# Kernel optimization log

Hardware: AMD Instinct MI355X
Metric: run time of the kernel (lower is better)

## Reference

```python
import jax, jax.numpy as jnp
import numpy as np

GRID_SIZE = 5
NUM_BASES = 2 ** GRID_SIZE - 1  # 31: actual number of Haar bases produced by the loop

def _haar_edges():
    left, mid, right = [], [], []
    for level in range(GRID_SIZE):
        scale = 2 ** level
        for shift in range(scale):
            left.append(shift / scale)
            mid.append((shift + 0.5) / scale)
            right.append((shift + 1.0) / scale)
    return (np.asarray(left, np.float32), np.asarray(mid, np.float32), np.asarray(right, np.float32))

_LEFT, _MID, _RIGHT = _haar_edges()


def setup_inputs() -> dict:
    key = jax.random.key(0)
    k1, k2, k3 = jax.random.split(key, 3)
    B, IN, OUT = 16384, 256, 256
    x = jax.random.normal(k1, (B, IN), dtype=jnp.float32)
    base_weight = jax.random.normal(k2, (OUT, IN), dtype=jnp.float32) * 0.05
    spline_weight = jax.random.normal(k3, (OUT, IN, NUM_BASES), dtype=jnp.float32) * 0.05
    spline_scaler = jnp.ones((OUT, IN), dtype=jnp.float32)
    return {"x": x, "base_weight": base_weight, "spline_weight": spline_weight, "spline_scaler": spline_scaler}


def reference(x, base_weight, spline_weight, spline_scaler):
    # per-feature min/max normalization over the batch dim
    x_min = jnp.min(x, axis=0, keepdims=True)
    x_max = jnp.max(x, axis=0, keepdims=True)
    xn = (x - x_min) / (x_max - x_min + 1e-8)            # [B, IN]
    left = jnp.asarray(_LEFT, x.dtype)
    mid = jnp.asarray(_MID, x.dtype)
    right = jnp.asarray(_RIGHT, x.dtype)
    xe = xn[..., None]                                    # [B, IN, 1]
    mask1 = ((xe >= left) & (xe < mid)).astype(x.dtype)
    mask2 = ((xe >= mid) & (xe < right)).astype(x.dtype)
    bases = mask1 - mask2                                 # [B, IN, NB]
    base_out = jax.nn.relu(x) @ base_weight.T             # [B, OUT]
    sw = spline_weight * spline_scaler[..., None]         # [OUT, IN, NB]
    wavelet_out = jnp.einsum('bik,oik->bo', bases, sw)    # [B, OUT]
    return base_out + wavelet_out
```

## Files before the change

kernel.cpp:

```cpp
#include <hip/hip_runtime.h>
#include <stdint.h>

typedef short s16x8 __attribute__((ext_vector_type(8)));
typedef float f32x4 __attribute__((ext_vector_type(4)));

#define IN_F   256
#define OUT_F  256
#define BATCH  16384
#define NB     31
#define KONE   8192
#define KTOT   8448

typedef const __attribute__((address_space(1))) void* as1cvp;
typedef __attribute__((address_space(3))) void* as3vp;

__device__ __forceinline__ unsigned short f2bf(float f) {
    unsigned u = __float_as_uint(f);
    u += 0x7FFFu + ((u >> 16) & 1u);
    return (unsigned short)(u >> 16);
}
__device__ __forceinline__ unsigned fkey(float f) {
    unsigned b = __float_as_uint(f);
    return (b & 0x80000000u) ? ~b : (b | 0x80000000u);
}
__device__ __forceinline__ float funkey(unsigned k) {
    return __uint_as_float((k & 0x80000000u) ? (k & 0x7FFFFFFFu) : ~k);
}

__global__ void minmax_atomic(const float* __restrict__ x,
                              unsigned* __restrict__ pminP, unsigned* __restrict__ pmaxP) {
    const int t = threadIdx.x;
    const int b0 = blockIdx.x * 32;
    float mn = 3.4e38f, mx = -3.4e38f;
    for (int r = 0; r < 32; ++r) {
        float v = x[(size_t)(b0 + r) * IN_F + t];
        mn = fminf(mn, v);
        mx = fmaxf(mx, v);
    }
    atomicMin(&pminP[t], fkey(mn));
    atomicMax(&pmaxP[t], fkey(mx));
}

__global__ void build_wb(const float* __restrict__ bw, const float* __restrict__ sw,
                         const float* __restrict__ sc, unsigned short* __restrict__ Wb) {
    const int o = blockIdx.x;
    const int k0 = blockIdx.y * 2112;
    const int t = threadIdx.x;
    for (int k = k0 + t; k < k0 + 2112; k += 256) {
        float val;
        if (k < KONE) {
            int i = k >> 5, j = k & 31;
            float s = sc[o * IN_F + i];
            float acc = 0.f;
#pragma unroll
            for (int l = 0; l < 5; ++l) {
                int kk = (1 << l) - 1 + (j >> (5 - l));
                float w = sw[((size_t)(o * IN_F + i)) * NB + kk];
                acc += (((j >> (4 - l)) & 1) ? -w : w);
            }
            val = acc * s;
        } else {
            val = bw[o * IN_F + (k - KONE)];
        }
        Wb[(size_t)o * KTOT + k] = f2bf(val);
    }
}

__global__ __launch_bounds__(256) void leafk_t(
    const float* __restrict__ x, const unsigned* __restrict__ pminP,
    const unsigned* __restrict__ pmaxP, unsigned char* __restrict__ lt) {
    __shared__ unsigned char lsh[256 * 68];
    __shared__ float xminsh[IN_F], rdensh[IN_F];
    const int t = threadIdx.x;
    const int b0 = blockIdx.x * 64;
    {
        float mn = funkey(pminP[t]), mx = funkey(pmaxP[t]);
        xminsh[t] = mn;
        rdensh[t] = 1.0f / (mx - mn + 1e-8f);
    }
    __syncthreads();
    const float xmn = xminsh[t], rdn = rdensh[t];
    for (int r = 0; r < 64; ++r) {
        float v = x[(size_t)(b0 + r) * IN_F + t];
        float xn = (v - xmn) * rdn;
        int l = (int)(xn * 32.0f);
        lsh[t * 68 + r] = (l >= 0 && l < 32) ? (unsigned char)l : (unsigned char)255;
    }
    __syncthreads();
    const int lane = t & 63, w = t >> 6;
    const unsigned* lshU = (const unsigned*)lsh;
#pragma unroll
    for (int ib = 0; ib < 16; ++ib) {
        int i = ib * 16 + w * 4 + (lane >> 4);
        unsigned val = lshU[i * 17 + (lane & 15)];
        *(unsigned*)(lt + (size_t)i * BATCH + b0 + (lane & 15) * 4) = val;
    }
}

__global__ __launch_bounds__(128, 2) void gemm_kan(
    const float* __restrict__ x,
    const unsigned short* __restrict__ Wb,
    const unsigned char* __restrict__ lt,
    float* __restrict__ out)
{
    __shared__ unsigned short Ash[64 * 64];
    __shared__ unsigned short Bsh[2 * 64 * 64];

    const int t     = threadIdx.x;
    const int lane  = t & 63;
    const int wv    = t >> 6;
    const int mtile = blockIdx.x;
    const int ntile = blockIdx.y;

    {
        uint4 z; z.x = z.y = z.z = z.w = 0u;
        uint4* a4 = (uint4*)Ash;
#pragma unroll
        for (int r = 0; r < 4; ++r) a4[t + r * 128] = z;
    }

    const unsigned char* bbase = (const unsigned char*)(Wb
        + (size_t)(ntile * 64 + wv * 32 + (lane >> 3)) * KTOT
        + (((lane & 7) ^ (lane >> 3)) << 3));

    const int am = t >> 1;
    const int ag = t & 1;
    const size_t lrow0 = (size_t)mtile * 64;
    int ps = -1;

    unsigned char lf = lt[(size_t)ag * BATCH + lrow0 + am];

#pragma unroll
    for (int q = 0; q < 4; ++q)
        __builtin_amdgcn_global_load_lds(
            (as1cvp)(bbase + (size_t)q * 8 * KTOT * 2),
            (as3vp)(uint32_t)(uintptr_t)(Bsh + wv * 2048 + q * 512), 16, 0, 0);
    __syncthreads();

    f32x4 acc[2][4] = {};
    const int rr = lane & 15, kq = lane >> 4;

    for (int kb = 0; kb < 132; ++kb) {
        const int cur = kb & 1;
        if (kb < 128) {
            if (ps >= 0) Ash[ps] = 0;
            int l = lf;
            if (l < 32) {
                int c = (ag << 2) + (l >> 3);
                ps = (am << 6) + ((c ^ (am & 7)) << 3) + (l & 7);
                Ash[ps] = 0x3F80;
            } else ps = -1;
        } else {
            const float* xr = x + (size_t)(mtile * 64 + wv * 32) * IN_F + (kb - 128) * 64 + lane;
            const int cslot = (lane >> 3);
#pragma unroll
            for (int m0 = 0; m0 < 32; ++m0) {
                int m = wv * 32 + m0;
                float v = xr[(size_t)m0 * IN_F];
                Ash[(m << 6) + ((cslot ^ (m & 7)) << 3) + (lane & 7)] = f2bf(fmaxf(v, 0.0f));
            }
        }
        __syncthreads();

        if (kb + 1 < 132) {
            const unsigned char* src = bbase + (size_t)(kb + 1) * 128;
            unsigned short* dst = Bsh + (1 - cur) * 4096 + wv * 2048;
#pragma unroll
            for (int q = 0; q < 4; ++q)
                __builtin_amdgcn_global_load_lds(
                    (as1cvp)(src + (size_t)q * 8 * KTOT * 2),
                    (as3vp)(uint32_t)(uintptr_t)(dst + q * 512), 16, 0, 0);
        }
        if (kb + 1 < 128) {
            lf = lt[(size_t)((kb + 1) * 2 + ag) * BATCH + lrow0 + am];
        }

        const unsigned short* bb = Bsh + cur * 4096;
#pragma unroll
        for (int ks = 0; ks < 2; ++ks) {
            const int c = (ks << 2) + kq;
            s16x8 af[2], bfr[4];
#pragma unroll
            for (int mt = 0; mt < 2; ++mt) {
                int m = wv * 32 + mt * 16 + rr;
                af[mt] = *(const s16x8*)&Ash[(m << 6) + ((c ^ (m & 7)) << 3)];
            }
#pragma unroll
            for (int nt = 0; nt < 4; ++nt) {
                int n = nt * 16 + rr;
                bfr[nt] = *(const s16x8*)&bb[(n << 6) + ((c ^ (n & 7)) << 3)];
            }
#pragma unroll
            for (int mt = 0; mt < 2; ++mt)
#pragma unroll
                for (int nt = 0; nt < 4; ++nt)
                    acc[mt][nt] = __builtin_amdgcn_mfma_f32_16x16x32_bf16(
                        af[mt], bfr[nt], acc[mt][nt], 0, 0, 0);
        }
        __syncthreads();
    }

    const int rq = lane >> 4;
#pragma unroll
    for (int mt = 0; mt < 2; ++mt)
#pragma unroll
        for (int nt = 0; nt < 4; ++nt)
#pragma unroll
            for (int v = 0; v < 4; ++v) {
                int row = mtile * 64 + wv * 32 + mt * 16 + rq * 4 + v;
                int col = ntile * 64 + nt * 16 + rr;
                out[(size_t)row * OUT_F + col] = acc[mt][nt][v];
            }
}

extern "C" void kernel_launch(void* const* d_in, const int* in_sizes, int n_in,
                              void* d_out, int out_size, void* d_ws, size_t ws_size,
                              hipStream_t stream) {
    (void)in_sizes; (void)n_in; (void)out_size; (void)ws_size;
    const float* x  = (const float*)d_in[0];
    const float* bw = (const float*)d_in[1];
    const float* sw = (const float*)d_in[2];
    const float* sc = (const float*)d_in[3];
    float* out = (float*)d_out;

    char* ws = (char*)d_ws;
    unsigned short* Wb   = (unsigned short*)ws;
    unsigned char*  lt   = (unsigned char*)(ws + 4325376);
    unsigned*       pminP = (unsigned*)(ws + 8519680);
    unsigned*       pmaxP = (unsigned*)(ws + 8520704);

    hipMemsetAsync(pminP, 0xFF, 1024, stream);
    hipMemsetAsync(pmaxP, 0x00, 1024, stream);

    minmax_atomic<<<512, 256, 0, stream>>>(x, pminP, pmaxP);
    build_wb<<<dim3(256, 4), 256, 0, stream>>>(bw, sw, sc, Wb);
    leafk_t<<<256, 256, 0, stream>>>(x, pminP, pmaxP, lt);
    gemm_kan<<<dim3(256, 4), 128, 0, stream>>>(x, Wb, lt, out);
}
```

Before: 179.6 us.

## Build one-hot A fragments in registers, split K across blocks with atomics

The GEMM no longer stages the one-hot A matrix in shared memory. Each lane builds its bf16 one-hot fragment directly in registers from the leaf index, and the ReLU(x) part is loaded straight from global memory into registers. The K dimension is split over two blocks per output tile, with results accumulated into a zeroed output through float atomicAdd, and occupancy is raised to 4 blocks per SIMD. The atomic min/max over batch is replaced by a two-pass partial reduction that writes per-block partials into the workspace area later used by the leaf table. This adds an output memset and atomic traffic, and the summation order becomes nondeterministic.

```diff
diff --git a/kernel.cpp b/kernel.cpp
--- a/kernel.cpp
+++ b/kernel.cpp
@@ -19,16 +19,9 @@
     u += 0x7FFFu + ((u >> 16) & 1u);
     return (unsigned short)(u >> 16);
 }
-__device__ __forceinline__ unsigned fkey(float f) {
-    unsigned b = __float_as_uint(f);
-    return (b & 0x80000000u) ? ~b : (b | 0x80000000u);
-}
-__device__ __forceinline__ float funkey(unsigned k) {
-    return __uint_as_float((k & 0x80000000u) ? (k & 0x7FFFFFFFu) : ~k);
-}
-
-__global__ void minmax_atomic(const float* __restrict__ x,
-                              unsigned* __restrict__ pminP, unsigned* __restrict__ pmaxP) {
+
+__global__ void minmax_part(const float* __restrict__ x,
+                            float* __restrict__ pmn, float* __restrict__ pmx) {
     const int t = threadIdx.x;
     const int b0 = blockIdx.x * 32;
     float mn = 3.4e38f, mx = -3.4e38f;
@@ -37,8 +30,31 @@
         mn = fminf(mn, v);
         mx = fmaxf(mx, v);
     }
-    atomicMin(&pminP[t], fkey(mn));
-    atomicMax(&pmaxP[t], fkey(mx));
+    pmn[blockIdx.x * 256 + t] = mn;
+    pmx[blockIdx.x * 256 + t] = mx;
+}
+
+__global__ __launch_bounds__(64) void minmax_reduce(
+    const float* __restrict__ pmn, const float* __restrict__ pmx,
+    float* __restrict__ xminF, float* __restrict__ rdenF) {
+    const int j = blockIdx.x;
+    const int lane = threadIdx.x;
+    float mn = 3.4e38f, mx = -3.4e38f;
+#pragma unroll
+    for (int i = 0; i < 8; ++i) {
+        int b = lane * 8 + i;
+        mn = fminf(mn, pmn[(size_t)b * 256 + j]);
+        mx = fmaxf(mx, pmx[(size_t)b * 256 + j]);
+    }
+#pragma unroll
+    for (int off = 32; off; off >>= 1) {
+        mn = fminf(mn, __shfl_down(mn, off));
+        mx = fmaxf(mx, __shfl_down(mx, off));
+    }
+    if (lane == 0) {
+        xminF[j] = mn;
+        rdenF[j] = 1.0f / (mx - mn + 1e-8f);
+    }
 }
 
 __global__ void build_wb(const float* __restrict__ bw, const float* __restrict__ sw,
@@ -67,19 +83,12 @@
 }
 
 __global__ __launch_bounds__(256) void leafk_t(
-    const float* __restrict__ x, const unsigned* __restrict__ pminP,
-    const unsigned* __restrict__ pmaxP, unsigned char* __restrict__ lt) {
+    const float* __restrict__ x, const float* __restrict__ xminF,
+    const float* __restrict__ rdenF, unsigned char* __restrict__ lt) {
     __shared__ unsigned char lsh[256 * 68];
-    __shared__ float xminsh[IN_F], rdensh[IN_F];
     const int t = threadIdx.x;
     const int b0 = blockIdx.x * 64;
-    {
-        float mn = funkey(pminP[t]), mx = funkey(pmaxP[t]);
-        xminsh[t] = mn;
-        rdensh[t] = 1.0f / (mx - mn + 1e-8f);
-    }
-    __syncthreads();
-    const float xmn = xminsh[t], rdn = rdensh[t];
+    const float xmn = xminF[t], rdn = rdenF[t];
     for (int r = 0; r < 64; ++r) {
         float v = x[(size_t)(b0 + r) * IN_F + t];
         float xn = (v - xmn) * rdn;
@@ -97,13 +106,12 @@
     }
 }
 
-__global__ __launch_bounds__(128, 2) void gemm_kan(
+__global__ __launch_bounds__(128, 4) void gemm_kan(
     const float* __restrict__ x,
     const unsigned short* __restrict__ Wb,
     const unsigned char* __restrict__ lt,
     float* __restrict__ out)
 {
-    __shared__ unsigned short Ash[64 * 64];
     __shared__ unsigned short Bsh[2 * 64 * 64];
 
     const int t     = threadIdx.x;
@@ -111,58 +119,48 @@
     const int wv    = t >> 6;
     const int mtile = blockIdx.x;
     const int ntile = blockIdx.y;
-
-    {
-        uint4 z; z.x = z.y = z.z = z.w = 0u;
-        uint4* a4 = (uint4*)Ash;
-#pragma unroll
-        for (int r = 0; r < 4; ++r) a4[t + r * 128] = z;
-    }
+    const int kbeg  = blockIdx.z * 66;
+    const int kend  = kbeg + 66;
 
     const unsigned char* bbase = (const unsigned char*)(Wb
         + (size_t)(ntile * 64 + wv * 32 + (lane >> 3)) * KTOT
         + (((lane & 7) ^ (lane >> 3)) << 3));
 
-    const int am = t >> 1;
-    const int ag = t & 1;
-    const size_t lrow0 = (size_t)mtile * 64;
-    int ps = -1;
-
-    unsigned char lf = lt[(size_t)ag * BATCH + lrow0 + am];
-
-#pragma unroll
-    for (int q = 0; q < 4; ++q)
-        __builtin_amdgcn_global_load_lds(
-            (as1cvp)(bbase + (size_t)q * 8 * KTOT * 2),
-            (as3vp)(uint32_t)(uintptr_t)(Bsh + wv * 2048 + q * 512), 16, 0, 0);
+    const int rr = lane & 15, kq = lane >> 4;
+    const size_t lrow0 = (size_t)mtile * 64 + wv * 32 + rr;
+
+    int boff[2][4];
+#pragma unroll
+    for (int ks = 0; ks < 2; ++ks)
+#pragma unroll
+        for (int nt = 0; nt < 4; ++nt) {
+            int n = nt * 16 + rr, c = ks * 4 + kq;
+            boff[ks][nt] = (n << 7) + ((c ^ (n & 7)) << 4);
+        }
+
+    {
+        unsigned short* dst = Bsh + (kbeg & 1) * 4096 + wv * 2048;
+        const unsigned char* src = bbase + (size_t)kbeg * 128;
+#pragma unroll
+        for (int q = 0; q < 4; ++q)
+            __builtin_amdgcn_global_load_lds(
+                (as1cvp)(src + (size_t)q * 8 * KTOT * 2),
+                (as3vp)(uint32_t)(uintptr_t)(dst + q * 512), 16, 0, 0);
+    }
+    int lf[2][2];
+#pragma unroll
+    for (int ks = 0; ks < 2; ++ks)
+#pragma unroll
+        for (int mt = 0; mt < 2; ++mt)
+            lf[ks][mt] = lt[(size_t)(kbeg * 2 + ks) * BATCH + lrow0 + mt * 16];
     __syncthreads();
 
     f32x4 acc[2][4] = {};
-    const int rr = lane & 15, kq = lane >> 4;
-
-    for (int kb = 0; kb < 132; ++kb) {
+
+    for (int kb = kbeg; kb < kend; ++kb) {
         const int cur = kb & 1;
-        if (kb < 128) {
-            if (ps >= 0) Ash[ps] = 0;
-            int l = lf;
-            if (l < 32) {
-                int c = (ag << 2) + (l >> 3);
-                ps = (am << 6) + ((c ^ (am & 7)) << 3) + (l & 7);
-                Ash[ps] = 0x3F80;
-            } else ps = -1;
-        } else {
-            const float* xr = x + (size_t)(mtile * 64 + wv * 32) * IN_F + (kb - 128) * 64 + lane;
-            const int cslot = (lane >> 3);
-#pragma unroll
-            for (int m0 = 0; m0 < 32; ++m0) {
-                int m = wv * 32 + m0;
-                float v = xr[(size_t)m0 * IN_F];
-                Ash[(m << 6) + ((cslot ^ (m & 7)) << 3) + (lane & 7)] = f2bf(fmaxf(v, 0.0f));
-            }
-        }
-        __syncthreads();
-
-        if (kb + 1 < 132) {
+
+        if (kb + 1 < kend) {
             const unsigned char* src = bbase + (size_t)(kb + 1) * 128;
             unsigned short* dst = Bsh + (1 - cur) * 4096 + wv * 2048;
 #pragma unroll
@@ -171,31 +169,58 @@
                     (as1cvp)(src + (size_t)q * 8 * KTOT * 2),
                     (as3vp)(uint32_t)(uintptr_t)(dst + q * 512), 16, 0, 0);
         }
-        if (kb + 1 < 128) {
-            lf = lt[(size_t)((kb + 1) * 2 + ag) * BATCH + lrow0 + am];
-        }
-
-        const unsigned short* bb = Bsh + cur * 4096;
+
+        s16x8 af[2][2];
+        if (kb < 128) {
+#pragma unroll
+            for (int ks = 0; ks < 2; ++ks)
+#pragma unroll
+                for (int mt = 0; mt < 2; ++mt) {
+                    int L = lf[ks][mt];
+                    unsigned hot = ((L >> 3) == kq) ? (0x3F80u << ((L & 1) << 4)) : 0u;
+                    int slot = (L >> 1) & 3;
+                    union { s16x8 v; unsigned u[4]; } a;
+                    a.u[0] = (slot == 0) ? hot : 0u;
+                    a.u[1] = (slot == 1) ? hot : 0u;
+                    a.u[2] = (slot == 2) ? hot : 0u;
+                    a.u[3] = (slot == 3) ? hot : 0u;
+                    af[ks][mt] = a.v;
+                }
+        } else {
+#pragma unroll
+            for (int ks = 0; ks < 2; ++ks)
+#pragma unroll
+                for (int mt = 0; mt < 2; ++mt) {
+                    const float* xr = x + (lrow0 + mt * 16) * IN_F
+                                        + (kb - 128) * 64 + ks * 32 + kq * 8;
+                    union { s16x8 v; unsigned short s[8]; } a;
+#pragma unroll
+                    for (int e = 0; e < 8; ++e) a.s[e] = f2bf(fmaxf(xr[e], 0.0f));
+                    af[ks][mt] = a.v;
+                }
+        }
+
+        if (kb + 1 < kend && kb + 1 < 128) {
+#pragma unroll
+            for (int ks = 0; ks < 2; ++ks)
+#pragma unroll
+                for (int mt = 0; mt < 2; ++mt)
+                    lf[ks][mt] = lt[(size_t)((kb + 1) * 2 + ks) * BATCH + lrow0 + mt * 16];
+        }
+
+        const char* bb = (const char*)Bsh + cur * 8192;
 #pragma unroll
         for (int ks = 0; ks < 2; ++ks) {
-            const int c = (ks << 2) + kq;
-            s16x8 af[2], bfr[4];
-#pragma unroll
-            for (int mt = 0; mt < 2; ++mt) {
-                int m = wv * 32 + mt * 16 + rr;
-                af[mt] = *(const s16x8*)&Ash[(m << 6) + ((c ^ (m & 7)) << 3)];
-            }
-#pragma unroll
-            for (int nt = 0; nt < 4; ++nt) {
-                int n = nt * 16 + rr;
-                bfr[nt] = *(const s16x8*)&bb[(n << 6) + ((c ^ (n & 7)) << 3)];
-            }
+            s16x8 bfr[4];
+#pragma unroll
+            for (int nt = 0; nt < 4; ++nt)
+                bfr[nt] = *(const s16x8*)(bb + boff[ks][nt]);
 #pragma unroll
             for (int mt = 0; mt < 2; ++mt)
 #pragma unroll
                 for (int nt = 0; nt < 4; ++nt)
                     acc[mt][nt] = __builtin_amdgcn_mfma_f32_16x16x32_bf16(
-                        af[mt], bfr[nt], acc[mt][nt], 0, 0, 0);
+                        af[ks][mt], bfr[nt], acc[mt][nt], 0, 0, 0);
         }
         __syncthreads();
     }
@@ -209,7 +234,7 @@
             for (int v = 0; v < 4; ++v) {
                 int row = mtile * 64 + wv * 32 + mt * 16 + rq * 4 + v;
                 int col = ntile * 64 + nt * 16 + rr;
-                out[(size_t)row * OUT_F + col] = acc[mt][nt][v];
+                atomicAdd(&out[(size_t)row * OUT_F + col], acc[mt][nt][v]);
             }
 }
 
@@ -226,14 +251,16 @@
     char* ws = (char*)d_ws;
     unsigned short* Wb   = (unsigned short*)ws;
     unsigned char*  lt   = (unsigned char*)(ws + 4325376);
-    unsigned*       pminP = (unsigned*)(ws + 8519680);
-    unsigned*       pmaxP = (unsigned*)(ws + 8520704);
-
-    hipMemsetAsync(pminP, 0xFF, 1024, stream);
-    hipMemsetAsync(pmaxP, 0x00, 1024, stream);
-
-    minmax_atomic<<<512, 256, 0, stream>>>(x, pminP, pmaxP);
+    float* pmn   = (float*)(ws + 4325376);
+    float* pmx   = (float*)(ws + 4325376 + 524288);
+    float* xminF = (float*)(ws + 8519680);
+    float* rdenF = (float*)(ws + 8520704);
+
+    hipMemsetAsync(out, 0, (size_t)BATCH * OUT_F * 4, stream);
+
+    minmax_part<<<512, 256, 0, stream>>>(x, pmn, pmx);
+    minmax_reduce<<<256, 64, 0, stream>>>(pmn, pmx, xminF, rdenF);
     build_wb<<<dim3(256, 4), 256, 0, stream>>>(bw, sw, sc, Wb);
-    leafk_t<<<256, 256, 0, stream>>>(x, pminP, pmaxP, lt);
-    gemm_kan<<<dim3(256, 4), 128, 0, stream>>>(x, Wb, lt, out);
-}
+    leafk_t<<<256, 256, 0, stream>>>(x, xminF, rdenF, lt);
+    gemm_kan<<<dim3(256, 4, 2), 128, 0, stream>>>(x, Wb, lt, out);
+}
```

Result: no change. 178.4 us (-0.7%).
